# Kernel tuning notes

Measured on AMD Instinct MI355X. Metric: run time of the kernel, lower is better.

## Reference

```python
import jax, jax.numpy as jnp
import numpy as np

B, S, D = 16, 2048, 400
HEADS, HEAD_SIZE = 4, 100
SCALE = 1.0 / np.float32(100.0 ** 0.5)


def setup_inputs() -> dict:
    key = jax.random.key(0)
    ks = jax.random.split(key, 8)
    return {
        "x": jax.random.normal(ks[0], (B, S, D), jnp.float32),
        "attn_kernel": jax.random.normal(ks[1], (3, D, HEAD_SIZE), jnp.float32) * 0.05,
        "attn_dense": jax.random.normal(ks[2], (D, HEADS * HEAD_SIZE), jnp.float32) * 0.05,
        "d1_w": jax.random.normal(ks[3], (400, 400), jnp.float32) * 0.05,
        "d1_b": jnp.zeros((400,), jnp.float32),
        "fc1_w": jax.random.normal(ks[4], (800, 512), jnp.float32) * 0.05,
        "fc1_b": jnp.zeros((512,), jnp.float32),
        "fc2_w": jax.random.normal(ks[5], (512, 256), jnp.float32) * 0.05,
        "fc2_b": jnp.zeros((256,), jnp.float32),
    }


def reference(x, attn_kernel, attn_dense, d1_w, d1_b, fc1_w, fc1_b, fc2_w, fc2_b):
    # Multi-head attention. NOTE: the original loops `heads` times over the SAME
    # shared kernel, so all 4 head outputs are identical; compute once, tile.
    WQ = jnp.einsum('bsd,dh->bsh', x, attn_kernel[0])  # [B,S,100]
    WK = jnp.einsum('bsd,dh->bsh', x, attn_kernel[1])
    WV = jnp.einsum('bsd,dh->bsh', x, attn_kernel[2])
    scores = jnp.einsum('bqh,bkh->bqk', WQ, WK) * SCALE  # [B,S,S]
    probs = jax.nn.softmax(scores, axis=-1)
    V = jnp.einsum('bqk,bkh->bqh', probs, WV)  # [B,S,100]
    out = jnp.tile(V, (1, 1, HEADS))  # concat of identical heads -> [B,S,400]
    out = jnp.einsum('bsd,de->bse', out, attn_dense)  # [B,S,400]
    # Dropout layers are identity at inference.
    h = jax.nn.relu(jnp.einsum('bsd,de->bse', out, d1_w) + d1_b)  # [B,S,400]
    pooled = jnp.concatenate([jnp.max(h, axis=1), jnp.mean(h, axis=1)], axis=-1)  # [B,800]
    h = jax.nn.relu(pooled @ fc1_w + fc1_b)  # [B,512]
    h = jax.nn.relu(h @ fc2_w + fc2_b)  # [B,256]
    return h
```

## Files before the change

kernel.cpp:

```cpp
#include <hip/hip_runtime.h>

typedef __attribute__((ext_vector_type(8))) _Float16 f16x8;
typedef __attribute__((ext_vector_type(4))) float f4v;
typedef __attribute__((ext_vector_type(8))) unsigned short us8;
typedef __attribute__((ext_vector_type(4))) unsigned short us4;
typedef unsigned short u16;

__device__ __forceinline__ u16 h2b(_Float16 h) { return __builtin_bit_cast(u16, h); }
__device__ __forceinline__ float b2f(u16 b) {
    return (float)__builtin_bit_cast(_Float16, b);
}

#define BAR() do { asm volatile("s_waitcnt lgkmcnt(0)" ::: "memory"); \
                   __builtin_amdgcn_s_barrier(); } while (0)

__global__ void k_w2p(const float* __restrict__ ad, const float* __restrict__ d1w,
                      float* __restrict__ w2p) {
    int i = blockIdx.x * 256 + threadIdx.x;
    if (i >= 51200) return;
    int es = blockIdx.y;
    int d = i / 400, j = i % 400;
    float acc = 0.f;
    if (d < 100) {
        const float* a0 = ad + d * 400 + es * 100;
        const float* wr = d1w + (es * 100) * 400 + j;
        #pragma unroll 4
        for (int e = 0; e < 100; ++e) {
            float av = a0[e] + a0[40000 + e] + a0[80000 + e] + a0[120000 + e];
            acc += av * wr[e * 400];
        }
    }
    w2p[es * 51200 + i] = acc;
}

__global__ void k_w2r(const float* __restrict__ w2p, u16* __restrict__ w2f) {
    int i = blockIdx.x * 256 + threadIdx.x;
    if (i >= 51200) return;
    float acc = w2p[i] + w2p[51200 + i] + w2p[102400 + i] + w2p[153600 + i];
    int d = i / 400, j = i % 400;
    int idx = ((j >> 4) * 4 + (d >> 5)) * 512 + (((d >> 3) & 3) * 16 + (j & 15)) * 8 + (d & 7);
    w2f[idx] = h2b((_Float16)acc);
}

__global__ void k_wprep(const float* __restrict__ ak, u16* __restrict__ wsp) {
    int i = blockIdx.x * 256 + threadIdx.x;
    if (i >= 159744) return;
    int k = i & 31, n = (i >> 5) & 127;
    int xx = i >> 12;
    int ks = xx % 13, m = xx / 13;
    int gk = ks * 32 + k;
    float v = (n < 100 && gk < 400) ? ak[m * 40000 + gk * 100 + n] : 0.f;
    _Float16 hb = (_Float16)v;
    _Float16 lb = (_Float16)(v - (float)hb);
    long base = (long)xx * 8192;
    int pos = n * 32 + ((((k >> 3) ^ (n & 3)) << 3) | (k & 7));
    wsp[base + pos] = h2b(hb);
    wsp[base + 4096 + pos] = h2b(lb);
}

__global__ __launch_bounds__(512) void k_gemm_qkv(
    const float* __restrict__ x, const u16* __restrict__ wsp,
    u16* __restrict__ QH, u16* __restrict__ KH, u16* __restrict__ VT) {
    __shared__ __align__(16) u16 smem[49152];

    const int tid = threadIdx.x;
    const int rowblk = blockIdx.x;
    const long row0 = (long)rowblk * 128;
    const int w = tid >> 6, l = tid & 63, g = l >> 4, c15 = l & 15;
    const int sr = tid >> 2, skc = tid & 3;

    f4v aQ[8], aK[8], aV[8];
    #pragma unroll
    for (int nt = 0; nt < 8; ++nt) {
        aQ[nt] = (f4v){0.f, 0.f, 0.f, 0.f};
        aK[nt] = (f4v){0.f, 0.f, 0.f, 0.f};
        aV[nt] = (f4v){0.f, 0.f, 0.f, 0.f};
    }

    const u16* wq  = wsp;
    const u16* wkh = wsp + 106496;
    const u16* wkl = wsp + 110592;
    const u16* wv  = wsp + 212992;

    float4 xr0, xr1;
    us8 wr[4];
    const int xpos = sr * 32 + ((skc * 8) ^ ((sr & 3) << 3));

    {
        const float* xp = x + (row0 + sr) * 400 + skc * 8;
        xr0 = *(const float4*)xp;
        xr1 = *(const float4*)(xp + 4);
        wr[0] = *(const us8*)&wq [(long)tid * 8];
        wr[1] = *(const us8*)&wkh[(long)tid * 8];
        wr[2] = *(const us8*)&wkl[(long)tid * 8];
        wr[3] = *(const us8*)&wv [(long)tid * 8];
        float va[8] = {xr0.x, xr0.y, xr0.z, xr0.w, xr1.x, xr1.y, xr1.z, xr1.w};
        us8 hi8, lo8;
        #pragma unroll
        for (int j = 0; j < 8; ++j) {
            _Float16 h = (_Float16)va[j];
            hi8[j] = h2b(h);
            lo8[j] = h2b((_Float16)(va[j] - (float)h));
        }
        *(us8*)&smem[xpos] = hi8;
        *(us8*)&smem[4096 + xpos] = lo8;
        *(us8*)&smem[8192  + tid * 8] = wr[0];
        *(us8*)&smem[12288 + tid * 8] = wr[1];
        *(us8*)&smem[16384 + tid * 8] = wr[2];
        *(us8*)&smem[20480 + tid * 8] = wr[3];
        const float* xp1 = x + (row0 + sr) * 400 + 32 + skc * 8;
        xr0 = *(const float4*)xp1;
        xr1 = *(const float4*)(xp1 + 4);
        wr[0] = *(const us8*)&wq [8192 + (long)tid * 8];
        wr[1] = *(const us8*)&wkh[8192 + (long)tid * 8];
        wr[2] = *(const us8*)&wkl[8192 + (long)tid * 8];
        wr[3] = *(const us8*)&wv [8192 + (long)tid * 8];
    }

    for (int ks = 0; ks < 13; ++ks) {
        BAR();
        u16* cb = smem + (ks & 1) * 24576;
        u16* sb = smem + ((ks & 1) ^ 1) * 24576;
        if (ks + 1 < 13) {
            float va[8] = {xr0.x, xr0.y, xr0.z, xr0.w, xr1.x, xr1.y, xr1.z, xr1.w};
            us8 hi8, lo8;
            #pragma unroll
            for (int j = 0; j < 8; ++j) {
                _Float16 h = (_Float16)va[j];
                hi8[j] = h2b(h);
                lo8[j] = h2b((_Float16)(va[j] - (float)h));
            }
            *(us8*)&sb[xpos] = hi8;
            *(us8*)&sb[4096 + xpos] = lo8;
            *(us8*)&sb[8192  + tid * 8] = wr[0];
            *(us8*)&sb[12288 + tid * 8] = wr[1];
            *(us8*)&sb[16384 + tid * 8] = wr[2];
            *(us8*)&sb[20480 + tid * 8] = wr[3];
            if (ks + 2 < 13) {
                if ((ks + 2) * 32 + skc * 8 < 400) {
                    const float* xp = x + (row0 + sr) * 400 + (ks + 2) * 32 + skc * 8;
                    xr0 = *(const float4*)xp;
                    xr1 = *(const float4*)(xp + 4);
                } else {
                    xr0 = make_float4(0.f, 0.f, 0.f, 0.f);
                    xr1 = make_float4(0.f, 0.f, 0.f, 0.f);
                }
                long wo = (long)(ks + 2) * 8192 + (long)tid * 8;
                wr[0] = *(const us8*)&wq [wo];
                wr[1] = *(const us8*)&wkh[wo];
                wr[2] = *(const us8*)&wkl[wo];
                wr[3] = *(const us8*)&wv [wo];
            }
        }
        const int arow = w * 16 + c15;
        const int axo = arow * 32 + ((g * 8) ^ ((arow & 3) << 3));
        f16x8 ah = *(const f16x8*)&cb[axo];
        f16x8 al = *(const f16x8*)&cb[4096 + axo];
        __builtin_amdgcn_s_setprio(1);
        #pragma unroll
        for (int nt = 0; nt < 8; ++nt) {
            int brow = nt * 16 + c15;
            int boff = brow * 32 + ((g * 8) ^ ((brow & 3) << 3));
            f16x8 qb = *(const f16x8*)&cb[8192 + boff];
            aQ[nt] = __builtin_amdgcn_mfma_f32_16x16x32_f16(ah, qb, aQ[nt], 0, 0, 0);
            aQ[nt] = __builtin_amdgcn_mfma_f32_16x16x32_f16(al, qb, aQ[nt], 0, 0, 0);
            f16x8 kh = *(const f16x8*)&cb[12288 + boff];
            aK[nt] = __builtin_amdgcn_mfma_f32_16x16x32_f16(ah, kh, aK[nt], 0, 0, 0);
            aK[nt] = __builtin_amdgcn_mfma_f32_16x16x32_f16(al, kh, aK[nt], 0, 0, 0);
            f16x8 kl = *(const f16x8*)&cb[16384 + boff];
            aK[nt] = __builtin_amdgcn_mfma_f32_16x16x32_f16(ah, kl, aK[nt], 0, 0, 0);
            f16x8 vb = *(const f16x8*)&cb[20480 + boff];
            aV[nt] = __builtin_amdgcn_mfma_f32_16x16x32_f16(ah, vb, aV[nt], 0, 0, 0);
            aV[nt] = __builtin_amdgcn_mfma_f32_16x16x32_f16(al, vb, aV[nt], 0, 0, 0);
        }
        __builtin_amdgcn_s_setprio(0);
    }
    BAR();
    u16* epi = smem;

    {
        const float qs = 0.14426950408889634f;
        #pragma unroll
        for (int nt = 0; nt < 8; ++nt) {
            #pragma unroll
            for (int r = 0; r < 4; ++r) {
                int row = w * 16 + 4 * g + r, col = nt * 16 + c15;
                epi[row * 128 + (col ^ ((row & 7) << 3))] =
                    h2b((_Float16)(aQ[nt][r] * qs));
            }
        }
        __syncthreads();
        #pragma unroll
        for (int r = 0; r < 4; ++r) {
            int u = tid + r * 512;
            int row = u >> 4, c = u & 15;
            *(us8*)&QH[(row0 + row) * 128 + c * 8] =
                *(const us8*)&epi[row * 128 + ((c * 8) ^ ((row & 7) << 3))];
        }
        __syncthreads();
    }
    {
        #pragma unroll
        for (int nt = 0; nt < 8; ++nt) {
            #pragma unroll
            for (int r = 0; r < 4; ++r) {
                int row = w * 16 + 4 * g + r, col = nt * 16 + c15;
                epi[row * 128 + (col ^ ((row & 7) << 3))] = h2b((_Float16)aK[nt][r]);
            }
        }
        __syncthreads();
        u16* dst = KH + (long)rowblk * 16384;
        #pragma unroll
        for (int r = 0; r < 4; ++r) {
            int u = tid + r * 512;
            *(us8*)&dst[(long)u * 8] = *(const us8*)&epi[u * 8];
        }
        __syncthreads();
    }
    {
        const int q0 = w * 16 + 4 * g;
        const int vtile = q0 >> 6, q0w = q0 & 63;
        #pragma unroll
        for (int nt = 0; nt < 8; ++nt) {
            int d = nt * 16 + c15;
            if (d < 112) {
                us4 v4;
                #pragma unroll
                for (int r = 0; r < 4; ++r) v4[r] = h2b((_Float16)aV[nt][r]);
                *(us4*)&epi[vtile * 8192 + d * 64 + (q0w ^ ((d & 7) << 3))] = v4;
            }
        }
        __syncthreads();
        #pragma unroll
        for (int r = 0; r < 4; ++r) {
            int u = tid + r * 512;
            int vt2 = u >> 10, uu = u & 1023;
            if (uu < 896)
                *(us8*)&VT[((long)(2 * rowblk + vt2)) * 7168 + (long)uu * 8] =
                    *(const us8*)&epi[u * 8];
        }
    }
}

__global__ __launch_bounds__(512) void k_flash(
    const u16* __restrict__ Qg, const u16* __restrict__ Kg,
    const u16* __restrict__ Vg, u16* __restrict__ VOI,
    float* __restrict__ ML) {
    __shared__ __align__(16) char KS[2][16384];
    __shared__ __align__(16) char VS[2][14336];
    __shared__ __align__(16) char PS[8][2048];

    const int tid = threadIdx.x;
    const int w = tid >> 6, l = tid & 63, g = l >> 4, c15 = l & 15;
    const int b = blockIdx.y, qt = blockIdx.x, half = blockIdx.z;
    const int t0 = half * 16;

    const u16* qp = Qg + ((long)b * 2048 + qt * 128 + w * 16 + c15) * 128;
    f16x8 qh[4];
    #pragma unroll
    for (int ks = 0; ks < 4; ++ks) qh[ks] = *(const f16x8*)(qp + ks * 32 + g * 8);

    f4v O[7];
    #pragma unroll
    for (int i = 0; i < 7; ++i) O[i] = (f4v){0.f, 0.f, 0.f, 0.f};
    float lrow = 0.f;

    const char* Kb = (const char*)(Kg + (long)b * 32 * 8192);
    const char* Vb = (const char*)(Vg + (long)b * 32 * 7168);
    char* Pw = PS[w];

    us8 kreg[2], vreg[2];
    #pragma unroll
    for (int r = 0; r < 2; ++r) {
        int u = tid + r * 512;
        kreg[r] = *(const us8*)(Kb + (long)t0 * 16384 + (long)u * 16);
        if (u < 896) vreg[r] = *(const us8*)(Vb + (long)t0 * 14336 + (long)u * 16);
    }
    #pragma unroll
    for (int r = 0; r < 2; ++r) {
        int u = tid + r * 512;
        *(us8*)(KS[0] + u * 16) = kreg[r];
        if (u < 896) *(us8*)(VS[0] + u * 16) = vreg[r];
    }
    #pragma unroll
    for (int r = 0; r < 2; ++r) {
        int u = tid + r * 512;
        kreg[r] = *(const us8*)(Kb + (long)(t0 + 1) * 16384 + (long)u * 16);
        if (u < 896) vreg[r] = *(const us8*)(Vb + (long)(t0 + 1) * 14336 + (long)u * 16);
    }

    for (int t = t0; t < t0 + 16; ++t) {
        const int cur = (t - t0) & 1;
        BAR();
        if (t + 1 < t0 + 16) {
            #pragma unroll
            for (int r = 0; r < 2; ++r) {
                int u = tid + r * 512;
                *(us8*)(KS[cur ^ 1] + u * 16) = kreg[r];
                if (u < 896) *(us8*)(VS[cur ^ 1] + u * 16) = vreg[r];
            }
            if (t + 2 < t0 + 16) {
                #pragma unroll
                for (int r = 0; r < 2; ++r) {
                    int u = tid + r * 512;
                    kreg[r] = *(const us8*)(Kb + (long)(t + 2) * 16384 + (long)u * 16);
                    if (u < 896)
                        vreg[r] = *(const us8*)(Vb + (long)(t + 2) * 14336 + (long)u * 16);
                }
            }
        }
        const char* Kc = KS[cur];
        const char* Vc = VS[cur];

        f4v s[4];
        #pragma unroll
        for (int nt = 0; nt < 4; ++nt) s[nt] = (f4v){0.f, 0.f, 0.f, 0.f};
        __builtin_amdgcn_s_setprio(1);
        #pragma unroll
        for (int ks = 0; ks < 4; ++ks) {
            #pragma unroll
            for (int nt = 0; nt < 4; ++nt) {
                int key = nt * 16 + c15;
                f16x8 kf = *(const f16x8*)(Kc + key * 256 +
                                           ((ks * 64 + g * 16) ^ ((key & 7) << 4)));
                s[nt] = __builtin_amdgcn_mfma_f32_16x16x32_f16(kf, qh[ks], s[nt], 0, 0, 0);
            }
        }
        __builtin_amdgcn_s_setprio(0);

        float sum = 0.f;
        #pragma unroll
        for (int nt = 0; nt < 4; ++nt) {
            #pragma unroll
            for (int r = 0; r < 4; ++r) {
                float p = exp2f(s[nt][r]);
                s[nt][r] = p;
                sum += p;
            }
        }
        sum += __shfl_xor(sum, 16);
        sum += __shfl_xor(sum, 32);
        lrow += sum;

        #pragma unroll
        for (int nt = 0; nt < 4; ++nt) {
            uint2 pw2;
            pw2.x = __builtin_bit_cast(unsigned int,
                        __builtin_amdgcn_cvt_pkrtz(s[nt][0], s[nt][1]));
            pw2.y = __builtin_bit_cast(unsigned int,
                        __builtin_amdgcn_cvt_pkrtz(s[nt][2], s[nt][3]));
            *(uint2*)(Pw + c15 * 128 + ((32 * nt + 8 * g) ^ ((c15 & 7) << 4))) = pw2;
        }
        __builtin_amdgcn_s_setprio(1);
        #pragma unroll
        for (int k0 = 0; k0 < 2; ++k0) {
            f16x8 pa = *(const f16x8*)(Pw + c15 * 128 +
                                       ((k0 * 64 + g * 16) ^ ((c15 & 7) << 4)));
            #pragma unroll
            for (int dt = 0; dt < 7; ++dt) {
                int d = dt * 16 + c15;
                f16x8 vf = *(const f16x8*)(Vc + d * 128 +
                                           ((k0 * 64 + g * 16) ^ ((d & 7) << 4)));
                O[dt] = __builtin_amdgcn_mfma_f32_16x16x32_f16(pa, vf, O[dt], 0, 0, 0);
            }
        }
        __builtin_amdgcn_s_setprio(0);
    }

    if (g == 0) {
        ((float*)Pw)[c15] = lrow;
        ML[half * 32768 + b * 2048 + qt * 128 + w * 16 + c15] = lrow;
    }
    float linv[4];
    #pragma unroll
    for (int r = 0; r < 4; ++r) linv[r] = 1.f / ((float*)Pw)[4 * g + r];
    u16* vout = VOI + ((long)(half * 16 + b) * 2048 + qt * 128 + w * 16) * 112;
    #pragma unroll
    for (int r = 0; r < 4; ++r) {
        int row = 4 * g + r;
        #pragma unroll
        for (int dt = 0; dt < 7; ++dt)
            vout[row * 112 + dt * 16 + c15] =
                h2b((_Float16)(O[dt][r] * linv[r]));
    }
}

__global__ __launch_bounds__(256) void k_hpool(
    const u16* __restrict__ VOI, const float* __restrict__ ML,
    const u16* __restrict__ W2F, const float* __restrict__ d1b,
    float* __restrict__ pmax, float* __restrict__ psum) {
    __shared__ __align__(16) u16 A[8192];
    __shared__ float redM[4][400], redS[4][400];
    __shared__ float wgt[64][2];
    const int tid = threadIdx.x;
    const int w = tid >> 6, l = tid & 63, g = l >> 4, c15 = l & 15;
    const int b = blockIdx.y, rt = blockIdx.x;

    if (tid < 64) {
        float a = ML[b * 2048 + rt * 64 + tid];
        float c = ML[32768 + b * 2048 + rt * 64 + tid];
        float inv = 1.f / (a + c);
        wgt[tid][0] = a * inv;
        wgt[tid][1] = c * inv;
    }
    if (tid < 128) {
        int r = tid >> 1, c = 14 + (tid & 1);
        us8 z = {0, 0, 0, 0, 0, 0, 0, 0};
        *(us8*)&A[r * 128 + ((c * 8) ^ ((r & 7) << 3))] = z;
    }
    __syncthreads();

    const u16* s1 = VOI + ((long)b * 2048 + rt * 64) * 112;
    const u16* s2 = VOI + ((long)(16 + b) * 2048 + rt * 64) * 112;
    #pragma unroll
    for (int r = 0; r < 4; ++r) {
        int u = tid + r * 256;
        if (u < 896) {
            int row = u / 14, c = u % 14;
            us8 p1 = *(const us8*)&s1[row * 112 + c * 8];
            us8 p2 = *(const us8*)&s2[row * 112 + c * 8];
            float w1 = wgt[row][0], w2 = wgt[row][1];
            us8 o;
            #pragma unroll
            for (int j = 0; j < 8; ++j)
                o[j] = h2b((_Float16)(w1 * b2f(p1[j]) + w2 * b2f(p2[j])));
            *(us8*)&A[row * 128 + ((c * 8) ^ ((row & 7) << 3))] = o;
        }
    }
    __syncthreads();

    const int arow = w * 16 + c15;
    f16x8 af[4];
    #pragma unroll
    for (int ks = 0; ks < 4; ++ks)
        af[ks] = *(const f16x8*)&A[arow * 128 + ((ks * 32 + g * 8) ^ ((arow & 7) << 3))];

    for (int nt = 0; nt < 25; ++nt) {
        f4v acc = (f4v){0.f, 0.f, 0.f, 0.f};
        #pragma unroll
        for (int ks = 0; ks < 4; ++ks) {
            f16x8 bf = *(const f16x8*)&W2F[(nt * 4 + ks) * 512 + l * 8];
            acc = __builtin_amdgcn_mfma_f32_16x16x32_f16(af[ks], bf, acc, 0, 0, 0);
        }
        float bias = d1b[nt * 16 + c15];
        float mx4 = -1e30f, sm4 = 0.f;
        #pragma unroll
        for (int r = 0; r < 4; ++r) {
            float h = fmaxf(acc[r] + bias, 0.f);
            mx4 = fmaxf(mx4, h);
            sm4 += h;
        }
        mx4 = fmaxf(mx4, __shfl_xor(mx4, 16));
        mx4 = fmaxf(mx4, __shfl_xor(mx4, 32));
        sm4 += __shfl_xor(sm4, 16);
        sm4 += __shfl_xor(sm4, 32);
        if (g == 0) {
            redM[w][nt * 16 + c15] = mx4;
            redS[w][nt * 16 + c15] = sm4;
        }
    }
    __syncthreads();
    for (int j = tid; j < 400; j += 256) {
        float mx = fmaxf(fmaxf(redM[0][j], redM[1][j]), fmaxf(redM[2][j], redM[3][j]));
        float sm = redS[0][j] + redS[1][j] + redS[2][j] + redS[3][j];
        pmax[((long)b * 32 + rt) * 400 + j] = mx;
        psum[((long)b * 32 + rt) * 400 + j] = sm;
    }
}

__global__ __launch_bounds__(256) void k_pred(
    const float* __restrict__ pmax, const float* __restrict__ psum,
    float* __restrict__ pooled) {
    __shared__ float rm[16][17], rs[16][17];
    const int b = blockIdx.x, jt = blockIdx.y, tid = threadIdx.x;
    const int jo = tid & 15, ts = tid >> 4;
    const int j = jt * 16 + jo;
    float mx = -1e30f, sm = 0.f;
    for (int t = ts; t < 32; t += 16) {
        mx = fmaxf(mx, pmax[((long)b * 32 + t) * 400 + j]);
        sm += psum[((long)b * 32 + t) * 400 + j];
    }
    rm[ts][jo] = mx; rs[ts][jo] = sm;
    __syncthreads();
    if (tid < 16) {
        float m2 = rm[0][tid], s2 = rs[0][tid];
        #pragma unroll
        for (int t = 1; t < 16; ++t) { m2 = fmaxf(m2, rm[t][tid]); s2 += rs[t][tid]; }
        pooled[b * 800 + jt * 16 + tid] = m2;
        pooled[b * 800 + 400 + jt * 16 + tid] = s2 * (1.f / 2048.f);
    }
}

__global__ __launch_bounds__(256) void k_fc1(
    const float* __restrict__ pooled, const float* __restrict__ w,
    const float* __restrict__ bias, float* __restrict__ out) {
    __shared__ float pl[800];
    __shared__ float red[16][17];
    const int b = blockIdx.x, jt = blockIdx.y, tid = threadIdx.x;
    const int jo = tid & 15, ks = tid >> 4;
    const int j = jt * 16 + jo;
    for (int i = tid; i < 800; i += 256) pl[i] = pooled[b * 800 + i];
    __syncthreads();
    float acc = 0.f;
    #pragma unroll 5
    for (int kk = 0; kk < 50; ++kk) {
        int k = ks * 50 + kk;
        acc += pl[k] * w[k * 512 + j];
    }
    red[ks][jo] = acc;
    __syncthreads();
    if (tid < 16) {
        float s = red[0][tid];
        #pragma unroll
        for (int t = 1; t < 16; ++t) s += red[t][tid];
        out[b * 512 + jt * 16 + tid] = fmaxf(s + bias[jt * 16 + tid], 0.f);
    }
}

__global__ __launch_bounds__(256) void k_fc2(
    const float* __restrict__ h, const float* __restrict__ w,
    const float* __restrict__ bias, float* __restrict__ out) {
    __shared__ float hl[512];
    __shared__ float red[16][17];
    const int b = blockIdx.x, jt = blockIdx.y, tid = threadIdx.x;
    const int jo = tid & 15, ks = tid >> 4;
    const int j = jt * 16 + jo;
    for (int i = tid; i < 512; i += 256) hl[i] = h[b * 512 + i];
    __syncthreads();
    float acc = 0.f;
    #pragma unroll 4
    for (int kk = 0; kk < 32; ++kk) {
        int k = ks * 32 + kk;
        acc += hl[k] * w[k * 256 + j];
    }
    red[ks][jo] = acc;
    __syncthreads();
    if (tid < 16) {
        float s = red[0][tid];
        #pragma unroll
        for (int t = 1; t < 16; ++t) s += red[t][tid];
        out[b * 256 + jt * 16 + tid] = fmaxf(s + bias[jt * 16 + tid], 0.f);
    }
}

extern "C" void kernel_launch(void* const* d_in, const int* in_sizes, int n_in,
                              void* d_out, int out_size, void* d_ws, size_t ws_size,
                              hipStream_t stream) {
    const float* x          = (const float*)d_in[0];
    const float* attn_kernel= (const float*)d_in[1];
    const float* attn_dense = (const float*)d_in[2];
    const float* d1_w       = (const float*)d_in[3];
    const float* d1_b       = (const float*)d_in[4];
    const float* fc1_w      = (const float*)d_in[5];
    const float* fc1_b      = (const float*)d_in[6];
    const float* fc2_w      = (const float*)d_in[7];
    const float* fc2_b      = (const float*)d_in[8];
    float* out = (float*)d_out;
    char*  wsb = (char*)d_ws;

    u16*    QH   = (u16*)(wsb);
    u16*    KH   = (u16*)(wsb + 8388608);
    u16*    VT   = (u16*)(wsb + 16777216);
    u16*    VOI  = (u16*)(wsb + 24117248);
    u16*    WSP  = (u16*)(wsb + 38797312);
    u16*    W2F  = (u16*)(wsb + 39436288);
    float*  PMAX = (float*)(wsb + 39538688);
    float*  PSUM = (float*)(wsb + 40357888);
    float*  ML   = (float*)(wsb + 41177088);
    float*  W2P  = (float*)(wsb + 41439232);
    float*  POOL = (float*)(wsb + 42258432);
    float*  FC1  = (float*)(wsb + 42309632);

    k_wprep<<<624, 256, 0, stream>>>(attn_kernel, WSP);
    k_w2p <<<dim3(200, 4), 256, 0, stream>>>(attn_dense, d1_w, W2P);
    k_w2r <<<200, 256, 0, stream>>>(W2P, W2F);
    k_gemm_qkv<<<256, 512, 0, stream>>>(x, WSP, QH, KH, VT);
    k_flash<<<dim3(16, 16, 2), 512, 0, stream>>>(QH, KH, VT, VOI, ML);
    k_hpool<<<dim3(32, 16), 256, 0, stream>>>(VOI, ML, W2F, d1_b, PMAX, PSUM);
    k_pred<<<dim3(16, 25), 256, 0, stream>>>(PMAX, PSUM, POOL);
    k_fc1 <<<dim3(16, 32), 256, 0, stream>>>(POOL, fc1_w, fc1_b, FC1);
    k_fc2 <<<dim3(16, 16), 256, 0, stream>>>(FC1, fc2_w, fc2_b, out);
}
```

Measured before the change: 137.2 us.

## Halve QKV GEMM row tile to 64 rows and split N across warps

Result: no change. 137.5 us (+0.2%).

```diff
diff --git a/kernel.cpp b/kernel.cpp
--- a/kernel.cpp
+++ b/kernel.cpp
@@ -61,20 +61,22 @@
 __global__ __launch_bounds__(512) void k_gemm_qkv(
     const float* __restrict__ x, const u16* __restrict__ wsp,
     u16* __restrict__ QH, u16* __restrict__ KH, u16* __restrict__ VT) {
-    __shared__ __align__(16) u16 smem[49152];
+    __shared__ __align__(16) u16 smem[40960];
 
     const int tid = threadIdx.x;
     const int rowblk = blockIdx.x;
-    const long row0 = (long)rowblk * 128;
+    const long row0 = (long)rowblk * 64;
     const int w = tid >> 6, l = tid & 63, g = l >> 4, c15 = l & 15;
-    const int sr = tid >> 2, skc = tid & 3;
-
-    f4v aQ[8], aK[8], aV[8];
-    #pragma unroll
-    for (int nt = 0; nt < 8; ++nt) {
-        aQ[nt] = (f4v){0.f, 0.f, 0.f, 0.f};
-        aK[nt] = (f4v){0.f, 0.f, 0.f, 0.f};
-        aV[nt] = (f4v){0.f, 0.f, 0.f, 0.f};
+    const int wm = w & 3, wn = w >> 2;
+    const int sr = (tid & 255) >> 2, skc = tid & 3;
+    const bool xload = tid < 256;
+
+    f4v aQ[4], aK[4], aV[4];
+    #pragma unroll
+    for (int j = 0; j < 4; ++j) {
+        aQ[j] = (f4v){0.f, 0.f, 0.f, 0.f};
+        aK[j] = (f4v){0.f, 0.f, 0.f, 0.f};
+        aV[j] = (f4v){0.f, 0.f, 0.f, 0.f};
     }
 
     const u16* wq  = wsp;
@@ -87,30 +89,36 @@
     const int xpos = sr * 32 + ((skc * 8) ^ ((sr & 3) << 3));
 
     {
-        const float* xp = x + (row0 + sr) * 400 + skc * 8;
-        xr0 = *(const float4*)xp;
-        xr1 = *(const float4*)(xp + 4);
+        if (xload) {
+            const float* xp = x + (row0 + sr) * 400 + skc * 8;
+            xr0 = *(const float4*)xp;
+            xr1 = *(const float4*)(xp + 4);
+        }
         wr[0] = *(const us8*)&wq [(long)tid * 8];
         wr[1] = *(const us8*)&wkh[(long)tid * 8];
         wr[2] = *(const us8*)&wkl[(long)tid * 8];
         wr[3] = *(const us8*)&wv [(long)tid * 8];
-        float va[8] = {xr0.x, xr0.y, xr0.z, xr0.w, xr1.x, xr1.y, xr1.z, xr1.w};
-        us8 hi8, lo8;
-        #pragma unroll
-        for (int j = 0; j < 8; ++j) {
-            _Float16 h = (_Float16)va[j];
-            hi8[j] = h2b(h);
-            lo8[j] = h2b((_Float16)(va[j] - (float)h));
-        }
-        *(us8*)&smem[xpos] = hi8;
-        *(us8*)&smem[4096 + xpos] = lo8;
-        *(us8*)&smem[8192  + tid * 8] = wr[0];
-        *(us8*)&smem[12288 + tid * 8] = wr[1];
-        *(us8*)&smem[16384 + tid * 8] = wr[2];
-        *(us8*)&smem[20480 + tid * 8] = wr[3];
-        const float* xp1 = x + (row0 + sr) * 400 + 32 + skc * 8;
-        xr0 = *(const float4*)xp1;
-        xr1 = *(const float4*)(xp1 + 4);
+        if (xload) {
+            float va[8] = {xr0.x, xr0.y, xr0.z, xr0.w, xr1.x, xr1.y, xr1.z, xr1.w};
+            us8 hi8, lo8;
+            #pragma unroll
+            for (int j = 0; j < 8; ++j) {
+                _Float16 h = (_Float16)va[j];
+                hi8[j] = h2b(h);
+                lo8[j] = h2b((_Float16)(va[j] - (float)h));
+            }
+            *(us8*)&smem[xpos] = hi8;
+            *(us8*)&smem[2048 + xpos] = lo8;
+        }
+        *(us8*)&smem[4096  + tid * 8] = wr[0];
+        *(us8*)&smem[8192  + tid * 8] = wr[1];
+        *(us8*)&smem[12288 + tid * 8] = wr[2];
+        *(us8*)&smem[16384 + tid * 8] = wr[3];
+        if (xload) {
+            const float* xp1 = x + (row0 + sr) * 400 + 32 + skc * 8;
+            xr0 = *(const float4*)xp1;
+            xr1 = *(const float4*)(xp1 + 4);
+        }
         wr[0] = *(const us8*)&wq [8192 + (long)tid * 8];
         wr[1] = *(const us8*)&wkh[8192 + (long)tid * 8];
         wr[2] = *(const us8*)&wkl[8192 + (long)tid * 8];
@@ -119,31 +127,35 @@
 
     for (int ks = 0; ks < 13; ++ks) {
         BAR();
-        u16* cb = smem + (ks & 1) * 24576;
-        u16* sb = smem + ((ks & 1) ^ 1) * 24576;
+        u16* cb = smem + (ks & 1) * 20480;
+        u16* sb = smem + ((ks & 1) ^ 1) * 20480;
         if (ks + 1 < 13) {
-            float va[8] = {xr0.x, xr0.y, xr0.z, xr0.w, xr1.x, xr1.y, xr1.z, xr1.w};
-            us8 hi8, lo8;
-            #pragma unroll
-            for (int j = 0; j < 8; ++j) {
-                _Float16 h = (_Float16)va[j];
-                hi8[j] = h2b(h);
-                lo8[j] = h2b((_Float16)(va[j] - (float)h));
-            }
-            *(us8*)&sb[xpos] = hi8;
-            *(us8*)&sb[4096 + xpos] = lo8;
-            *(us8*)&sb[8192  + tid * 8] = wr[0];
-            *(us8*)&sb[12288 + tid * 8] = wr[1];
-            *(us8*)&sb[16384 + tid * 8] = wr[2];
-            *(us8*)&sb[20480 + tid * 8] = wr[3];
+            if (xload) {
+                float va[8] = {xr0.x, xr0.y, xr0.z, xr0.w, xr1.x, xr1.y, xr1.z, xr1.w};
+                us8 hi8, lo8;
+                #pragma unroll
+                for (int j = 0; j < 8; ++j) {
+                    _Float16 h = (_Float16)va[j];
+                    hi8[j] = h2b(h);
+                    lo8[j] = h2b((_Float16)(va[j] - (float)h));
+                }
+                *(us8*)&sb[xpos] = hi8;
+                *(us8*)&sb[2048 + xpos] = lo8;
+            }
+            *(us8*)&sb[4096  + tid * 8] = wr[0];
+            *(us8*)&sb[8192  + tid * 8] = wr[1];
+            *(us8*)&sb[12288 + tid * 8] = wr[2];
+            *(us8*)&sb[16384 + tid * 8] = wr[3];
             if (ks + 2 < 13) {
-                if ((ks + 2) * 32 + skc * 8 < 400) {
-                    const float* xp = x + (row0 + sr) * 400 + (ks + 2) * 32 + skc * 8;
-                    xr0 = *(const float4*)xp;
-                    xr1 = *(const float4*)(xp + 4);
-                } else {
-                    xr0 = make_float4(0.f, 0.f, 0.f, 0.f);
-                    xr1 = make_float4(0.f, 0.f, 0.f, 0.f);
+                if (xload) {
+                    if ((ks + 2) * 32 + skc * 8 < 400) {
+                        const float* xp = x + (row0 + sr) * 400 + (ks + 2) * 32 + skc * 8;
+                        xr0 = *(const float4*)xp;
+                        xr1 = *(const float4*)(xp + 4);
+                    } else {
+                        xr0 = make_float4(0.f, 0.f, 0.f, 0.f);
+                        xr1 = make_float4(0.f, 0.f, 0.f, 0.f);
+                    }
                 }
                 long wo = (long)(ks + 2) * 8192 + (long)tid * 8;
                 wr[0] = *(const us8*)&wq [wo];
@@ -152,26 +164,26 @@
                 wr[3] = *(const us8*)&wv [wo];
             }
         }
-        const int arow = w * 16 + c15;
+        const int arow = wm * 16 + c15;
         const int axo = arow * 32 + ((g * 8) ^ ((arow & 3) << 3));
         f16x8 ah = *(const f16x8*)&cb[axo];
-        f16x8 al = *(const f16x8*)&cb[4096 + axo];
+        f16x8 al = *(const f16x8*)&cb[2048 + axo];
         __builtin_amdgcn_s_setprio(1);
         #pragma unroll
-        for (int nt = 0; nt < 8; ++nt) {
-            int brow = nt * 16 + c15;
+        for (int j = 0; j < 4; ++j) {
+            int brow = (wn * 4 + j) * 16 + c15;
             int boff = brow * 32 + ((g * 8) ^ ((brow & 3) << 3));
-            f16x8 qb = *(const f16x8*)&cb[8192 + boff];
-            aQ[nt] = __builtin_amdgcn_mfma_f32_16x16x32_f16(ah, qb, aQ[nt], 0, 0, 0);
-            aQ[nt] = __builtin_amdgcn_mfma_f32_16x16x32_f16(al, qb, aQ[nt], 0, 0, 0);
-            f16x8 kh = *(const f16x8*)&cb[12288 + boff];
-            aK[nt] = __builtin_amdgcn_mfma_f32_16x16x32_f16(ah, kh, aK[nt], 0, 0, 0);
-            aK[nt] = __builtin_amdgcn_mfma_f32_16x16x32_f16(al, kh, aK[nt], 0, 0, 0);
-            f16x8 kl = *(const f16x8*)&cb[16384 + boff];
-            aK[nt] = __builtin_amdgcn_mfma_f32_16x16x32_f16(ah, kl, aK[nt], 0, 0, 0);
-            f16x8 vb = *(const f16x8*)&cb[20480 + boff];
-            aV[nt] = __builtin_amdgcn_mfma_f32_16x16x32_f16(ah, vb, aV[nt], 0, 0, 0);
-            aV[nt] = __builtin_amdgcn_mfma_f32_16x16x32_f16(al, vb, aV[nt], 0, 0, 0);
+            f16x8 qb = *(const f16x8*)&cb[4096 + boff];
+            aQ[j] = __builtin_amdgcn_mfma_f32_16x16x32_f16(ah, qb, aQ[j], 0, 0, 0);
+            aQ[j] = __builtin_amdgcn_mfma_f32_16x16x32_f16(al, qb, aQ[j], 0, 0, 0);
+            f16x8 kh = *(const f16x8*)&cb[8192 + boff];
+            aK[j] = __builtin_amdgcn_mfma_f32_16x16x32_f16(ah, kh, aK[j], 0, 0, 0);
+            aK[j] = __builtin_amdgcn_mfma_f32_16x16x32_f16(al, kh, aK[j], 0, 0, 0);
+            f16x8 kl = *(const f16x8*)&cb[12288 + boff];
+            aK[j] = __builtin_amdgcn_mfma_f32_16x16x32_f16(ah, kl, aK[j], 0, 0, 0);
+            f16x8 vb = *(const f16x8*)&cb[16384 + boff];
+            aV[j] = __builtin_amdgcn_mfma_f32_16x16x32_f16(ah, vb, aV[j], 0, 0, 0);
+            aV[j] = __builtin_amdgcn_mfma_f32_16x16x32_f16(al, vb, aV[j], 0, 0, 0);
         }
         __builtin_amdgcn_s_setprio(0);
     }
@@ -181,17 +193,17 @@
     {
         const float qs = 0.14426950408889634f;
         #pragma unroll
-        for (int nt = 0; nt < 8; ++nt) {
+        for (int j = 0; j < 4; ++j) {
             #pragma unroll
             for (int r = 0; r < 4; ++r) {
-                int row = w * 16 + 4 * g + r, col = nt * 16 + c15;
+                int row = wm * 16 + 4 * g + r, col = (wn * 4 + j) * 16 + c15;
                 epi[row * 128 + (col ^ ((row & 7) << 3))] =
-                    h2b((_Float16)(aQ[nt][r] * qs));
+                    h2b((_Float16)(aQ[j][r] * qs));
             }
         }
         __syncthreads();
         #pragma unroll
-        for (int r = 0; r < 4; ++r) {
+        for (int r = 0; r < 2; ++r) {
             int u = tid + r * 512;
             int row = u >> 4, c = u & 15;
             *(us8*)&QH[(row0 + row) * 128 + c * 8] =
@@ -201,42 +213,40 @@
     }
     {
         #pragma unroll
-        for (int nt = 0; nt < 8; ++nt) {
+        for (int j = 0; j < 4; ++j) {
             #pragma unroll
             for (int r = 0; r < 4; ++r) {
-                int row = w * 16 + 4 * g + r, col = nt * 16 + c15;
-                epi[row * 128 + (col ^ ((row & 7) << 3))] = h2b((_Float16)aK[nt][r]);
+                int row = wm * 16 + 4 * g + r, col = (wn * 4 + j) * 16 + c15;
+                epi[row * 128 + (col ^ ((row & 7) << 3))] = h2b((_Float16)aK[j][r]);
             }
         }
         __syncthreads();
-        u16* dst = KH + (long)rowblk * 16384;
-        #pragma unroll
-        for (int r = 0; r < 4; ++r) {
+        u16* dst = KH + (long)rowblk * 8192;
+        #pragma unroll
+        for (int r = 0; r < 2; ++r) {
             int u = tid + r * 512;
             *(us8*)&dst[(long)u * 8] = *(const us8*)&epi[u * 8];
         }
         __syncthreads();
     }
     {
-        const int q0 = w * 16 + 4 * g;
-        const int vtile = q0 >> 6, q0w = q0 & 63;
-        #pragma unroll
-        for (int nt = 0; nt < 8; ++nt) {
-            int d = nt * 16 + c15;
+        const int q0 = wm * 16 + 4 * g;
+        #pragma unroll
+        for (int j = 0; j < 4; ++j) {
+            int d = (wn * 4 + j) * 16 + c15;
             if (d < 112) {
                 us4 v4;
                 #pragma unroll
-                for (int r = 0; r < 4; ++r) v4[r] = h2b((_Float16)aV[nt][r]);
-                *(us4*)&epi[vtile * 8192 + d * 64 + (q0w ^ ((d & 7) << 3))] = v4;
+                for (int r = 0; r < 4; ++r) v4[r] = h2b((_Float16)aV[j][r]);
+                *(us4*)&epi[d * 64 + (q0 ^ ((d & 7) << 3))] = v4;
             }
         }
         __syncthreads();
         #pragma unroll
-        for (int r = 0; r < 4; ++r) {
+        for (int r = 0; r < 2; ++r) {
             int u = tid + r * 512;
-            int vt2 = u >> 10, uu = u & 1023;
-            if (uu < 896)
-                *(us8*)&VT[((long)(2 * rowblk + vt2)) * 7168 + (long)uu * 8] =
+            if (u < 896)
+                *(us8*)&VT[(long)rowblk * 7168 + (long)u * 8] =
                     *(const us8*)&epi[u * 8];
         }
     }
@@ -574,7 +584,7 @@
     k_wprep<<<624, 256, 0, stream>>>(attn_kernel, WSP);
     k_w2p <<<dim3(200, 4), 256, 0, stream>>>(attn_dense, d1_w, W2P);
     k_w2r <<<200, 256, 0, stream>>>(W2P, W2F);
-    k_gemm_qkv<<<256, 512, 0, stream>>>(x, WSP, QH, KH, VT);
+    k_gemm_qkv<<<512, 512, 0, stream>>>(x, WSP, QH, KH, VT);
     k_flash<<<dim3(16, 16, 2), 512, 0, stream>>>(QH, KH, VT, VOI, ML);
     k_hpool<<<dim3(32, 16), 256, 0, stream>>>(VOI, ML, W2F, d1_b, PMAX, PSUM);
     k_pred<<<dim3(16, 25), 256, 0, stream>>>(PMAX, PSUM, POOL);
```
